# Kernel tuning notes

Measured on AMD Instinct MI355X. Metric: run time of the kernel, lower is better.

## Reference

```python
import jax, jax.numpy as jnp
import numpy as np

B = 32          # decode batch (one query token per sequence)
HID = 4096      # hidden_size
H = 32          # num_heads
D = 128         # head_dim
BLK = 16        # KV-cache block size (vLLM default)
MAXB = 64       # max blocks per sequence
NBLK = 2048     # total cache blocks
S = MAXB * BLK  # max context length = 1024
ROPE_THETA = 10000.0


def _rope(x, positions):
    # x: [B, H, D], positions: [B] int. GPT-NeoX / Llama half-split rotary.
    half = D // 2
    inv_freq = 1.0 / (ROPE_THETA ** (jnp.arange(0, half, dtype=jnp.float32) / half))
    freqs = positions.astype(jnp.float32)[:, None] * inv_freq[None, :]  # [B, D/2]
    cos = jnp.cos(freqs)[:, None, :]  # [B, 1, D/2]
    sin = jnp.sin(freqs)[:, None, :]
    x1, x2 = x[..., :half], x[..., half:]
    return jnp.concatenate([x1 * cos - x2 * sin, x1 * sin + x2 * cos], axis=-1)


def setup_inputs() -> dict:
    key = jax.random.key(0)
    ks = jax.random.split(key, 8)
    hidden_states = jax.random.normal(ks[0], (B, HID), jnp.float32)
    Wq = jax.random.normal(ks[1], (HID, HID), jnp.float32) * 0.02
    Wk = jax.random.normal(ks[2], (HID, HID), jnp.float32) * 0.02
    Wv = jax.random.normal(ks[3], (HID, HID), jnp.float32) * 0.02
    Wo = jax.random.normal(ks[4], (HID, HID), jnp.float32) * 0.02
    k_cache = jax.random.normal(ks[5], (NBLK, BLK, H, D), jnp.float32)
    v_cache = jax.random.normal(ks[6], (NBLK, BLK, H, D), jnp.float32)
    # each sequence owns MAXB distinct cache blocks (non-contiguous)
    block_tables = jax.random.permutation(ks[7], NBLK)[: B * MAXB].reshape(B, MAXB).astype(jnp.int32)
    context_lens = jax.random.randint(jax.random.fold_in(key, 9), (B,), S // 2, S + 1).astype(jnp.int32)
    positions = context_lens - 1  # current token position
    slot_mapping = (block_tables[jnp.arange(B), positions // BLK] * BLK + positions % BLK).astype(jnp.int32)
    return dict(hidden_states=hidden_states, k_cache=k_cache, v_cache=v_cache,
                Wq=Wq, Wk=Wk, Wv=Wv, Wo=Wo,
                positions=positions, slot_mapping=slot_mapping,
                block_tables=block_tables, context_lens=context_lens)


def reference(hidden_states, k_cache, v_cache, Wq, Wk, Wv, Wo,
              positions, slot_mapping, block_tables, context_lens):
    # QKV projections (bias-free, torch Linear convention: x @ W.T)
    q = (hidden_states @ Wq.T).reshape(B, H, D)
    k = (hidden_states @ Wk.T).reshape(B, H, D)
    v = (hidden_states @ Wv.T).reshape(B, H, D)
    q = _rope(q, positions)
    k = _rope(k, positions)
    # write new k/v into the paged cache at slot_mapping
    kc = k_cache.reshape(NBLK * BLK, H, D).at[slot_mapping].set(k)
    vc = v_cache.reshape(NBLK * BLK, H, D).at[slot_mapping].set(v)
    kc = kc.reshape(NBLK, BLK, H, D)
    vc = vc.reshape(NBLK, BLK, H, D)
    # paged gather: [B, MAXB, BLK, H, D] -> [B, S, H, D]
    keys = kc[block_tables].reshape(B, S, H, D)
    vals = vc[block_tables].reshape(B, S, H, D)
    scores = jnp.einsum('bhd,bshd->bhs', q, keys) * (D ** -0.5)
    valid = jnp.arange(S)[None, :] < context_lens[:, None]  # [B, S]
    scores = jnp.where(valid[:, None, :], scores, jnp.float32(-1e30))
    probs = jax.nn.softmax(scores, axis=-1)
    attn = jnp.einsum('bhs,bshd->bhd', probs, vals).reshape(B, H * D)
    return attn @ Wo.T
```

## Files before the change

kernel.cpp:

```cpp
#include <hip/hip_runtime.h>
#include <math.h>

#define HID 4096
#define B 32
#define H 32
#define D 128
#define KBLK 16
#define MAXB 64
#define CHUNK 128
#define NCHUNK 8

typedef float f4 __attribute__((ext_vector_type(4)));
#define NT_LD4(p) __builtin_nontemporal_load(reinterpret_cast<const f4*>(p))

template <int MODE>
__global__ __launch_bounds__(256) void gemv_kernel(
    const float* __restrict__ W0, const float* __restrict__ W1, const float* __restrict__ W2,
    const float* __restrict__ x, const int* __restrict__ positions, float* __restrict__ out)
{
    __shared__ float wt[8][256];
    __shared__ float buf[4][8][66];
    const int bid = blockIdx.x;
    const int mat = (MODE == 0) ? (bid >> 9) : 0;
    const int sub = bid & 511;
    const bool rope = (MODE == 0) && (mat < 2);
    const int head = sub >> 4;
    const int p0 = (sub & 15) << 2;
    const float* W = (mat == 0) ? W0 : ((mat == 1) ? W1 : W2);
    float* outp = out + (size_t)mat * (B * HID);

    const int tid = threadIdx.x;
    const int lane = tid & 63;
    const int wid = tid >> 6;
    const int b0 = wid << 3;

    float acc[8][8];
#pragma unroll
    for (int c = 0; c < 8; ++c)
#pragma unroll
        for (int j = 0; j < 8; ++j) acc[c][j] = 0.f;

    for (int k0 = 0; k0 < HID; k0 += 256) {
        __syncthreads();
#pragma unroll
        for (int i = 0; i < 2; ++i) {
            int idx = tid + (i << 8);
            int r = idx >> 6;
            int c4 = idx & 63;
            int cr = rope ? (head * 128 + p0 + (r & 3) + ((r >> 2) << 6))
                          : ((sub << 3) + r);
            f4 v = NT_LD4(&W[(size_t)cr * HID + k0 + (c4 << 2)]);
            *reinterpret_cast<f4*>(&wt[r][c4 << 2]) = v;
        }
        __syncthreads();

        float4 hs4[8];
#pragma unroll
        for (int j = 0; j < 8; ++j)
            hs4[j] = *reinterpret_cast<const float4*>(
                &x[(size_t)(b0 + j) * HID + k0 + (lane << 2)]);

#pragma unroll
        for (int c = 0; c < 8; ++c) {
            float4 w4 = *reinterpret_cast<const float4*>(&wt[c][lane << 2]);
#pragma unroll
            for (int j = 0; j < 8; ++j) {
                acc[c][j] += w4.x * hs4[j].x;
                acc[c][j] += w4.y * hs4[j].y;
                acc[c][j] += w4.z * hs4[j].z;
                acc[c][j] += w4.w * hs4[j].w;
            }
        }
    }

    float res[8];
#pragma unroll
    for (int c = 0; c < 8; ++c) {
#pragma unroll
        for (int j = 0; j < 8; ++j) buf[wid][j][lane] = acc[c][j];
        __builtin_amdgcn_sched_barrier(0);
        const float* rp = &buf[wid][lane >> 3][(lane & 7) << 3];
        float4 a = *reinterpret_cast<const float4*>(rp);
        float4 bb = *reinterpret_cast<const float4*>(rp + 4);
        __builtin_amdgcn_sched_barrier(0);
        float s = ((a.x + a.y) + (a.z + a.w)) + ((bb.x + bb.y) + (bb.z + bb.w));
        s += __shfl_xor(s, 1, 64);
        s += __shfl_xor(s, 2, 64);
        s += __shfl_xor(s, 4, 64);
        res[c] = s;
    }

    const int jme = lane >> 3;
    const int cme = lane & 7;
    float myv;
    if (rope) {
        const float pf = (float)positions[b0 + jme];
        float ro[8];
#pragma unroll
        for (int cc = 0; cc < 4; ++cc) {
            float invf = exp2f(-(float)(p0 + cc) * 0.20762050593046013f);
            float f = pf * invf;
            float cs = cosf(f), sn = sinf(f);
            ro[cc]     = res[cc] * cs - res[cc + 4] * sn;
            ro[cc + 4] = res[cc] * sn + res[cc + 4] * cs;
        }
        myv = ro[0];
#pragma unroll
        for (int cc = 1; cc < 8; ++cc) myv = (cme == cc) ? ro[cc] : myv;
    } else {
        myv = res[0];
#pragma unroll
        for (int cc = 1; cc < 8; ++cc) myv = (cme == cc) ? res[cc] : myv;
    }
    const int colw = rope ? (head * 128 + p0 + (cme & 3) + ((cme >> 2) << 6))
                          : ((sub << 3) + cme);
    outp[(size_t)(b0 + jme) * HID + colw] = myv;
}

__global__ __launch_bounds__(128) void attn_partial_kernel(
    const float* __restrict__ qkv,
    const float* __restrict__ k_cache,
    const float* __restrict__ v_cache,
    const int* __restrict__ block_tables,
    const int* __restrict__ context_lens,
    const int* __restrict__ positions,
    float* __restrict__ pm,
    float* __restrict__ pl,
    float* __restrict__ po)
{
    const int h = blockIdx.x;
    const int c = blockIdx.y;
    const int b = blockIdx.z;
    const int L = context_lens[b];
    const int s0 = c << 7;
    if (s0 >= L) return;
    const int Lc = min(L - s0, CHUNK);
    const int pos = positions[b];
    const int tid = threadIdx.x;

    __shared__ float sc[CHUNK];
    __shared__ float red[4];
    __shared__ int btl[8];
    __shared__ float o2[2][D];

    if (tid < 8) btl[tid] = block_tables[b * MAXB + (c << 3) + tid];
    __syncthreads();

    const float* qptr = qkv + (size_t)b * HID + h * D;
    const float* knew = qkv + (size_t)(B * HID) + (size_t)b * HID + h * D;
    const float* vnew = qkv + (size_t)(2 * B * HID) + (size_t)b * HID + h * D;
    const float scale = 0.088388347648318447f;

    const int hw = tid >> 5;
    const int hl = tid & 31;
    const float4 qv = *reinterpret_cast<const float4*>(qptr + (hl << 2));

    int i = hw;
    for (; i + 12 < Lc; i += 16) {
        const int sA = s0 + i, sB = sA + 4, sC = sA + 8, sD = sA + 12;
        const float* kp0 = (sA == pos) ? knew
            : k_cache + ((size_t)(btl[i >> 4] * KBLK + (sA & 15)) * H + h) * D;
        const float* kp1 = (sB == pos) ? knew
            : k_cache + ((size_t)(btl[(i + 4) >> 4] * KBLK + (sB & 15)) * H + h) * D;
        const float* kp2 = (sC == pos) ? knew
            : k_cache + ((size_t)(btl[(i + 8) >> 4] * KBLK + (sC & 15)) * H + h) * D;
        const float* kp3 = (sD == pos) ? knew
            : k_cache + ((size_t)(btl[(i + 12) >> 4] * KBLK + (sD & 15)) * H + h) * D;
        f4 k0 = NT_LD4(kp0 + (hl << 2));
        f4 k1 = NT_LD4(kp1 + (hl << 2));
        f4 k2 = NT_LD4(kp2 + (hl << 2));
        f4 k3 = NT_LD4(kp3 + (hl << 2));
        float d0 = qv.x * k0[0] + qv.y * k0[1] + qv.z * k0[2] + qv.w * k0[3];
        float d1 = qv.x * k1[0] + qv.y * k1[1] + qv.z * k1[2] + qv.w * k1[3];
        float d2 = qv.x * k2[0] + qv.y * k2[1] + qv.z * k2[2] + qv.w * k2[3];
        float d3 = qv.x * k3[0] + qv.y * k3[1] + qv.z * k3[2] + qv.w * k3[3];
#pragma unroll
        for (int m = 16; m; m >>= 1) {
            d0 += __shfl_xor(d0, m, 64);
            d1 += __shfl_xor(d1, m, 64);
            d2 += __shfl_xor(d2, m, 64);
            d3 += __shfl_xor(d3, m, 64);
        }
        if (hl == 0) {
            sc[i] = d0 * scale; sc[i + 4] = d1 * scale;
            sc[i + 8] = d2 * scale; sc[i + 12] = d3 * scale;
        }
    }
    for (; i < Lc; i += 4) {
        const int sA = s0 + i;
        const float* kp = (sA == pos) ? knew
            : k_cache + ((size_t)(btl[i >> 4] * KBLK + (sA & 15)) * H + h) * D;
        f4 k0 = NT_LD4(kp + (hl << 2));
        float d0 = qv.x * k0[0] + qv.y * k0[1] + qv.z * k0[2] + qv.w * k0[3];
#pragma unroll
        for (int m = 16; m; m >>= 1) d0 += __shfl_xor(d0, m, 64);
        if (hl == 0) sc[i] = d0 * scale;
    }
    for (; i < CHUNK; i += 4)
        if (hl == 0) sc[i] = -1e30f;
    __syncthreads();

    const int w = tid >> 6;
    const float xv = sc[tid];
    float m = xv;
#pragma unroll
    for (int mm = 32; mm; mm >>= 1) m = fmaxf(m, __shfl_xor(m, mm, 64));
    if ((tid & 63) == 0) red[w] = m;
    __syncthreads();
    const float gm = fmaxf(red[0], red[1]);

    float p = (xv > -1e29f) ? __expf(xv - gm) : 0.f;
    sc[tid] = p;
    float l = p;
#pragma unroll
    for (int mm = 32; mm; mm >>= 1) l += __shfl_xor(l, mm, 64);
    if ((tid & 63) == 0) red[2 + w] = l;
    __syncthreads();
    const float gl = red[2] + red[3];

    f4 oacc = {0.f, 0.f, 0.f, 0.f};
    i = hw;
    for (; i + 12 < Lc; i += 16) {
        const int sA = s0 + i, sB = sA + 4, sC = sA + 8, sD = sA + 12;
        const float* vp0 = (sA == pos) ? vnew
            : v_cache + ((size_t)(btl[i >> 4] * KBLK + (sA & 15)) * H + h) * D;
        const float* vp1 = (sB == pos) ? vnew
            : v_cache + ((size_t)(btl[(i + 4) >> 4] * KBLK + (sB & 15)) * H + h) * D;
        const float* vp2 = (sC == pos) ? vnew
            : v_cache + ((size_t)(btl[(i + 8) >> 4] * KBLK + (sC & 15)) * H + h) * D;
        const float* vp3 = (sD == pos) ? vnew
            : v_cache + ((size_t)(btl[(i + 12) >> 4] * KBLK + (sD & 15)) * H + h) * D;
        f4 v0 = NT_LD4(vp0 + (hl << 2));
        f4 v1 = NT_LD4(vp1 + (hl << 2));
        f4 v2 = NT_LD4(vp2 + (hl << 2));
        f4 v3 = NT_LD4(vp3 + (hl << 2));
        const float p0 = sc[i], p1 = sc[i + 4], p2 = sc[i + 8], p3 = sc[i + 12];
        oacc += p0 * v0;
        oacc += p1 * v1;
        oacc += p2 * v2;
        oacc += p3 * v3;
    }
    for (; i < Lc; i += 4) {
        const float* vp = (s0 + i == pos) ? vnew
            : v_cache + ((size_t)(btl[i >> 4] * KBLK + ((s0 + i) & 15)) * H + h) * D;
        f4 v0 = NT_LD4(vp + (hl << 2));
        oacc += sc[i] * v0;
    }
#pragma unroll
    for (int k = 0; k < 4; ++k) oacc[k] += __shfl_xor(oacc[k], 32, 64);
    if (hl < 32 && (tid < 32 || (tid >= 64 && tid < 96))) {
        *reinterpret_cast<f4*>(&o2[w][hl << 2]) = oacc;
    }
    __syncthreads();

    const int bh = b * H + h;
    {
        float o = o2[0][tid] + o2[1][tid];
        po[((size_t)bh * NCHUNK + c) * D + tid] = o;
    }
    if (tid == 0) {
        pm[bh * NCHUNK + c] = gm;
        pl[bh * NCHUNK + c] = gl;
    }
}

__global__ __launch_bounds__(128) void attn_combine_kernel(
    const float* __restrict__ pm, const float* __restrict__ pl,
    const float* __restrict__ po, const int* __restrict__ context_lens,
    float* __restrict__ attn_out)
{
    const int bh = blockIdx.x;
    const int b = bh >> 5;
    const int tid = threadIdx.x;
    const int nc = (context_lens[b] + CHUNK - 1) >> 7;

    float m = -1e30f;
    for (int c = 0; c < nc; ++c) m = fmaxf(m, pm[bh * NCHUNK + c]);
    float wsum = 0.f, o = 0.f;
    for (int c = 0; c < nc; ++c) {
        float wc = __expf(pm[bh * NCHUNK + c] - m);
        wsum += wc * pl[bh * NCHUNK + c];
        o += wc * po[((size_t)bh * NCHUNK + c) * D + tid];
    }
    attn_out[(size_t)bh * D + tid] = o / wsum;
}

extern "C" void kernel_launch(void* const* d_in, const int* in_sizes, int n_in,
                              void* d_out, int out_size, void* d_ws, size_t ws_size,
                              hipStream_t stream) {
    const float* hs        = (const float*)d_in[0];
    const float* k_cache   = (const float*)d_in[1];
    const float* v_cache   = (const float*)d_in[2];
    const float* Wq        = (const float*)d_in[3];
    const float* Wk        = (const float*)d_in[4];
    const float* Wv        = (const float*)d_in[5];
    const float* Wo        = (const float*)d_in[6];
    const int*   positions = (const int*)d_in[7];
    const int*   block_tables = (const int*)d_in[9];
    const int*   context_lens = (const int*)d_in[10];
    float* out = (float*)d_out;

    float* qkv     = (float*)d_ws;
    float* attn_ws = qkv + (size_t)3 * B * HID;
    float* pm      = attn_ws + (size_t)B * HID;
    float* pl      = pm + (size_t)B * H * NCHUNK;
    float* po      = pl + (size_t)B * H * NCHUNK;

    gemv_kernel<0><<<dim3(3 * 512), 256, 0, stream>>>(Wq, Wk, Wv, hs, positions, qkv);
    attn_partial_kernel<<<dim3(H, NCHUNK, B), 128, 0, stream>>>(
        qkv, k_cache, v_cache, block_tables, context_lens, positions, pm, pl, po);
    attn_combine_kernel<<<dim3(B * H), 128, 0, stream>>>(pm, pl, po, context_lens, attn_ws);
    gemv_kernel<1><<<dim3(512), 256, 0, stream>>>(Wo, Wo, Wo, attn_ws, positions, out);
}
```

Baseline: 246.2 us.

## Split-K output GEMV with atomics and process two heads per attention block

The output projection GEMV is split along K into two halves across 1024 blocks, with results accumulated via atomicAdd into a zero-initialised output. This doubles parallelism for the Wo stage. The attention partial kernel now handles two adjacent heads per block, so each wave reads a contiguous 1 KB span of the KV cache and does the softmax reduction per wave. The cost is an extra memset, float atomics (non-deterministic summation order) and half as many attention blocks.

```diff
diff --git a/kernel.cpp b/kernel.cpp
--- a/kernel.cpp
+++ b/kernel.cpp
@@ -23,6 +23,8 @@
     const int bid = blockIdx.x;
     const int mat = (MODE == 0) ? (bid >> 9) : 0;
     const int sub = bid & 511;
+    const int kbeg = (MODE == 1) ? ((bid >> 9) << 11) : 0;
+    const int kend = kbeg + ((MODE == 1) ? 2048 : 4096);
     const bool rope = (MODE == 0) && (mat < 2);
     const int head = sub >> 4;
     const int p0 = (sub & 15) << 2;
@@ -40,7 +42,7 @@
 #pragma unroll
         for (int j = 0; j < 8; ++j) acc[c][j] = 0.f;
 
-    for (int k0 = 0; k0 < HID; k0 += 256) {
+    for (int k0 = kbeg; k0 < kend; k0 += 256) {
         __syncthreads();
 #pragma unroll
         for (int i = 0; i < 2; ++i) {
@@ -114,7 +116,11 @@
     }
     const int colw = rope ? (head * 128 + p0 + (cme & 3) + ((cme >> 2) << 6))
                           : ((sub << 3) + cme);
-    outp[(size_t)(b0 + jme) * HID + colw] = myv;
+    if (MODE == 1) {
+        atomicAdd(&outp[(size_t)(b0 + jme) * HID + colw], myv);
+    } else {
+        outp[(size_t)(b0 + jme) * HID + colw] = myv;
+    }
 }
 
 __global__ __launch_bounds__(128) void attn_partial_kernel(
@@ -128,7 +134,7 @@
     float* __restrict__ pl,
     float* __restrict__ po)
 {
-    const int h = blockIdx.x;
+    const int h2 = blockIdx.x;
     const int c = blockIdx.y;
     const int b = blockIdx.z;
     const int L = context_lens[b];
@@ -138,38 +144,41 @@
     const int pos = positions[b];
     const int tid = threadIdx.x;
 
-    __shared__ float sc[CHUNK];
-    __shared__ float red[4];
+    __shared__ float sc[2][CHUNK];
+    __shared__ float mred[2], lred[2];
     __shared__ int btl[8];
-    __shared__ float o2[2][D];
+    __shared__ float o2[2][2][D];
 
     if (tid < 8) btl[tid] = block_tables[b * MAXB + (c << 3) + tid];
     __syncthreads();
 
-    const float* qptr = qkv + (size_t)b * HID + h * D;
-    const float* knew = qkv + (size_t)(B * HID) + (size_t)b * HID + h * D;
-    const float* vnew = qkv + (size_t)(2 * B * HID) + (size_t)b * HID + h * D;
+    const int w = tid >> 6;
+    const int l = tid & 63;
+    const int half = l >> 5;
+    const int hl = l & 31;
+
+    const float* qb   = qkv + (size_t)b * HID + h2 * 256;
+    const float* knew = qkv + (size_t)(B * HID) + (size_t)b * HID + h2 * 256;
+    const float* vnew = qkv + (size_t)(2 * B * HID) + (size_t)b * HID + h2 * 256;
     const float scale = 0.088388347648318447f;
 
-    const int hw = tid >> 5;
-    const int hl = tid & 31;
-    const float4 qv = *reinterpret_cast<const float4*>(qptr + (hl << 2));
-
-    int i = hw;
-    for (; i + 12 < Lc; i += 16) {
-        const int sA = s0 + i, sB = sA + 4, sC = sA + 8, sD = sA + 12;
+    const float4 qv = *reinterpret_cast<const float4*>(qb + (l << 2));
+
+    int i = w;
+    for (; i + 6 < Lc; i += 8) {
+        const int sA = s0 + i, sB = sA + 2, sC = sA + 4, sD = sA + 6;
         const float* kp0 = (sA == pos) ? knew
-            : k_cache + ((size_t)(btl[i >> 4] * KBLK + (sA & 15)) * H + h) * D;
+            : k_cache + (size_t)(btl[i >> 4] * KBLK + (sA & 15)) * (H * D) + h2 * 256;
         const float* kp1 = (sB == pos) ? knew
-            : k_cache + ((size_t)(btl[(i + 4) >> 4] * KBLK + (sB & 15)) * H + h) * D;
+            : k_cache + (size_t)(btl[(i + 2) >> 4] * KBLK + (sB & 15)) * (H * D) + h2 * 256;
         const float* kp2 = (sC == pos) ? knew
-            : k_cache + ((size_t)(btl[(i + 8) >> 4] * KBLK + (sC & 15)) * H + h) * D;
+            : k_cache + (size_t)(btl[(i + 4) >> 4] * KBLK + (sC & 15)) * (H * D) + h2 * 256;
         const float* kp3 = (sD == pos) ? knew
-            : k_cache + ((size_t)(btl[(i + 12) >> 4] * KBLK + (sD & 15)) * H + h) * D;
-        f4 k0 = NT_LD4(kp0 + (hl << 2));
-        f4 k1 = NT_LD4(kp1 + (hl << 2));
-        f4 k2 = NT_LD4(kp2 + (hl << 2));
-        f4 k3 = NT_LD4(kp3 + (hl << 2));
+            : k_cache + (size_t)(btl[(i + 6) >> 4] * KBLK + (sD & 15)) * (H * D) + h2 * 256;
+        f4 k0 = NT_LD4(kp0 + (l << 2));
+        f4 k1 = NT_LD4(kp1 + (l << 2));
+        f4 k2 = NT_LD4(kp2 + (l << 2));
+        f4 k3 = NT_LD4(kp3 + (l << 2));
         float d0 = qv.x * k0[0] + qv.y * k0[1] + qv.z * k0[2] + qv.w * k0[3];
         float d1 = qv.x * k1[0] + qv.y * k1[1] + qv.z * k1[2] + qv.w * k1[3];
         float d2 = qv.x * k2[0] + qv.y * k2[1] + qv.z * k2[2] + qv.w * k2[3];
@@ -182,85 +191,83 @@
             d3 += __shfl_xor(d3, m, 64);
         }
         if (hl == 0) {
-            sc[i] = d0 * scale; sc[i + 4] = d1 * scale;
-            sc[i + 8] = d2 * scale; sc[i + 12] = d3 * scale;
-        }
-    }
-    for (; i < Lc; i += 4) {
+            sc[half][i] = d0 * scale; sc[half][i + 2] = d1 * scale;
+            sc[half][i + 4] = d2 * scale; sc[half][i + 6] = d3 * scale;
+        }
+    }
+    for (; i < Lc; i += 2) {
         const int sA = s0 + i;
         const float* kp = (sA == pos) ? knew
-            : k_cache + ((size_t)(btl[i >> 4] * KBLK + (sA & 15)) * H + h) * D;
-        f4 k0 = NT_LD4(kp + (hl << 2));
+            : k_cache + (size_t)(btl[i >> 4] * KBLK + (sA & 15)) * (H * D) + h2 * 256;
+        f4 k0 = NT_LD4(kp + (l << 2));
         float d0 = qv.x * k0[0] + qv.y * k0[1] + qv.z * k0[2] + qv.w * k0[3];
 #pragma unroll
         for (int m = 16; m; m >>= 1) d0 += __shfl_xor(d0, m, 64);
-        if (hl == 0) sc[i] = d0 * scale;
-    }
-    for (; i < CHUNK; i += 4)
-        if (hl == 0) sc[i] = -1e30f;
+        if (hl == 0) sc[half][i] = d0 * scale;
+    }
+    for (; i < CHUNK; i += 2)
+        if (hl == 0) sc[half][i] = -1e30f;
     __syncthreads();
 
-    const int w = tid >> 6;
-    const float xv = sc[tid];
-    float m = xv;
-#pragma unroll
-    for (int mm = 32; mm; mm >>= 1) m = fmaxf(m, __shfl_xor(m, mm, 64));
-    if ((tid & 63) == 0) red[w] = m;
+    {
+        float x0 = sc[w][l], x1 = sc[w][l + 64];
+        float m = fmaxf(x0, x1);
+#pragma unroll
+        for (int mm = 32; mm; mm >>= 1) m = fmaxf(m, __shfl_xor(m, mm, 64));
+        float p0 = (x0 > -1e29f) ? __expf(x0 - m) : 0.f;
+        float p1 = (x1 > -1e29f) ? __expf(x1 - m) : 0.f;
+        sc[w][l] = p0; sc[w][l + 64] = p1;
+        float ls = p0 + p1;
+#pragma unroll
+        for (int mm = 32; mm; mm >>= 1) ls += __shfl_xor(ls, mm, 64);
+        if (l == 0) { mred[w] = m; lred[w] = ls; }
+    }
     __syncthreads();
-    const float gm = fmaxf(red[0], red[1]);
-
-    float p = (xv > -1e29f) ? __expf(xv - gm) : 0.f;
-    sc[tid] = p;
-    float l = p;
-#pragma unroll
-    for (int mm = 32; mm; mm >>= 1) l += __shfl_xor(l, mm, 64);
-    if ((tid & 63) == 0) red[2 + w] = l;
-    __syncthreads();
-    const float gl = red[2] + red[3];
 
     f4 oacc = {0.f, 0.f, 0.f, 0.f};
-    i = hw;
-    for (; i + 12 < Lc; i += 16) {
-        const int sA = s0 + i, sB = sA + 4, sC = sA + 8, sD = sA + 12;
+    i = w;
+    for (; i + 6 < Lc; i += 8) {
+        const int sA = s0 + i, sB = sA + 2, sC = sA + 4, sD = sA + 6;
         const float* vp0 = (sA == pos) ? vnew
-            : v_cache + ((size_t)(btl[i >> 4] * KBLK + (sA & 15)) * H + h) * D;
+            : v_cache + (size_t)(btl[i >> 4] * KBLK + (sA & 15)) * (H * D) + h2 * 256;
         const float* vp1 = (sB == pos) ? vnew
-            : v_cache + ((size_t)(btl[(i + 4) >> 4] * KBLK + (sB & 15)) * H + h) * D;
+            : v_cache + (size_t)(btl[(i + 2) >> 4] * KBLK + (sB & 15)) * (H * D) + h2 * 256;
         const float* vp2 = (sC == pos) ? vnew
-            : v_cache + ((size_t)(btl[(i + 8) >> 4] * KBLK + (sC & 15)) * H + h) * D;
+            : v_cache + (size_t)(btl[(i + 4) >> 4] * KBLK + (sC & 15)) * (H * D) + h2 * 256;
         const float* vp3 = (sD == pos) ? vnew
-            : v_cache + ((size_t)(btl[(i + 12) >> 4] * KBLK + (sD & 15)) * H + h) * D;
-        f4 v0 = NT_LD4(vp0 + (hl << 2));
-        f4 v1 = NT_LD4(vp1 + (hl << 2));
-        f4 v2 = NT_LD4(vp2 + (hl << 2));
-        f4 v3 = NT_LD4(vp3 + (hl << 2));
-        const float p0 = sc[i], p1 = sc[i + 4], p2 = sc[i + 8], p3 = sc[i + 12];
+            : v_cache + (size_t)(btl[(i + 6) >> 4] * KBLK + (sD & 15)) * (H * D) + h2 * 256;
+        f4 v0 = NT_LD4(vp0 + (l << 2));
+        f4 v1 = NT_LD4(vp1 + (l << 2));
+        f4 v2 = NT_LD4(vp2 + (l << 2));
+        f4 v3 = NT_LD4(vp3 + (l << 2));
+        const float p0 = sc[half][i], p1 = sc[half][i + 2];
+        const float p2 = sc[half][i + 4], p3 = sc[half][i + 6];
         oacc += p0 * v0;
         oacc += p1 * v1;
         oacc += p2 * v2;
         oacc += p3 * v3;
     }
-    for (; i < Lc; i += 4) {
+    for (; i < Lc; i += 2) {
         const float* vp = (s0 + i == pos) ? vnew
-            : v_cache + ((size_t)(btl[i >> 4] * KBLK + ((s0 + i) & 15)) * H + h) * D;
-        f4 v0 = NT_LD4(vp + (hl << 2));
-        oacc += sc[i] * v0;
-    }
-#pragma unroll
-    for (int k = 0; k < 4; ++k) oacc[k] += __shfl_xor(oacc[k], 32, 64);
-    if (hl < 32 && (tid < 32 || (tid >= 64 && tid < 96))) {
-        *reinterpret_cast<f4*>(&o2[w][hl << 2]) = oacc;
-    }
+            : v_cache + (size_t)(btl[i >> 4] * KBLK + ((s0 + i) & 15)) * (H * D) + h2 * 256;
+        f4 v0 = NT_LD4(vp + (l << 2));
+        oacc += sc[half][i] * v0;
+    }
+    *reinterpret_cast<f4*>(&o2[w][half][hl << 2]) = oacc;
     __syncthreads();
 
-    const int bh = b * H + h;
+    const int bh0 = b * H + 2 * h2;
     {
-        float o = o2[0][tid] + o2[1][tid];
-        po[((size_t)bh * NCHUNK + c) * D + tid] = o;
+        float oA = o2[0][0][tid] + o2[1][0][tid];
+        float oB = o2[0][1][tid] + o2[1][1][tid];
+        po[((size_t)bh0 * NCHUNK + c) * D + tid] = oA;
+        po[((size_t)(bh0 + 1) * NCHUNK + c) * D + tid] = oB;
     }
     if (tid == 0) {
-        pm[bh * NCHUNK + c] = gm;
-        pl[bh * NCHUNK + c] = gl;
+        pm[bh0 * NCHUNK + c] = mred[0];
+        pl[bh0 * NCHUNK + c] = lred[0];
+        pm[(bh0 + 1) * NCHUNK + c] = mred[1];
+        pl[(bh0 + 1) * NCHUNK + c] = lred[1];
     }
 }
 
@@ -306,9 +313,11 @@
     float* pl      = pm + (size_t)B * H * NCHUNK;
     float* po      = pl + (size_t)B * H * NCHUNK;
 
+    hipMemsetAsync(out, 0, (size_t)out_size * sizeof(float), stream);
+
     gemv_kernel<0><<<dim3(3 * 512), 256, 0, stream>>>(Wq, Wk, Wv, hs, positions, qkv);
-    attn_partial_kernel<<<dim3(H, NCHUNK, B), 128, 0, stream>>>(
+    attn_partial_kernel<<<dim3(H / 2, NCHUNK, B), 128, 0, stream>>>(
         qkv, k_cache, v_cache, block_tables, context_lens, positions, pm, pl, po);
     attn_combine_kernel<<<dim3(B * H), 128, 0, stream>>>(pm, pl, po, context_lens, attn_ws);
-    gemv_kernel<1><<<dim3(512), 256, 0, stream>>>(Wo, Wo, Wo, attn_ws, positions, out);
+    gemv_kernel<1><<<dim3(1024), 256, 0, stream>>>(Wo, Wo, Wo, attn_ws, positions, out);
 }
```

Result: slower. 254.4 us (+3.3%).
